# Optimization experiments

Hardware: AMD Instinct MI355X
Metric: run time of the kernel (lower is better)

The kernel has to match this reference:

```python
import jax, jax.numpy as jnp
import numpy as np

B, S, E = 4, 2048, 1024

def setup_inputs() -> dict:
    key = jax.random.key(0)
    ks = jax.random.split(key, 6)
    values = jax.random.normal(ks[0], (B, S, E), dtype=jnp.float32)
    keys_t = jax.random.normal(ks[1], (B, S, E), dtype=jnp.float32)
    query = jax.random.normal(ks[2], (B, S, E), dtype=jnp.float32)
    mask = jax.random.randint(ks[3], (B, 1, S), 0, 2, dtype=jnp.int32)
    W_out = jax.random.normal(ks[4], (E, E), dtype=jnp.float32) * (1.0 / np.sqrt(E))
    b_out = jax.random.normal(ks[5], (E,), dtype=jnp.float32) * 0.01
    return {"values": values, "keys": keys_t, "query": query, "mask": mask,
            "W_out": W_out, "b_out": b_out}

def reference(values, keys, query, mask, W_out, b_out):
    # scores: [B, S, S] = Q K^T / sqrt(embed_size)  (NOTE: module scales by
    # sqrt(embed_size), not sqrt(head_dim), and never applies q/k/v Linears)
    scale = 1.0 / jnp.sqrt(jnp.asarray(E, dtype=query.dtype))
    scores = jnp.einsum('bqe,bke->bqk', query, keys) * scale
    scores = jnp.where(mask == 0, -jnp.inf, scores)  # masked_fill(mask==0, -inf)
    attn = jax.nn.softmax(scores, axis=-1)
    out = jnp.einsum('bqk,bke->bqe', attn, values)
    # fc_out: torch Linear -> x @ W^T + b
    return out @ W_out.T + b_out
```

## Files before the change

kernel.cpp:

```cpp
#include <hip/hip_runtime.h>

#define BB 4
#define SS 2048
#define EE 1024

typedef _Float16 f16;
typedef _Float16 f16x4 __attribute__((ext_vector_type(4)));
typedef _Float16 f16x8 __attribute__((ext_vector_type(8)));
typedef float f32x4 __attribute__((ext_vector_type(4)));

typedef const __attribute__((address_space(1))) void* gas_ptr;
typedef __attribute__((address_space(3))) void* las_ptr;

__device__ __forceinline__ void gl_lds16(const void* g, void* l) {
  __builtin_amdgcn_global_load_lds((gas_ptr)g, (las_ptr)l, 16, 0, 0);
}

#define BAR() __builtin_amdgcn_s_barrier()
#define PRIO1() __builtin_amdgcn_s_setprio(1)
#define PRIO0() __builtin_amdgcn_s_setprio(0)
#define WAITV8() asm volatile("s_waitcnt vmcnt(8)" ::: "memory")
#define WAITV6() asm volatile("s_waitcnt vmcnt(6)" ::: "memory")
#define WAITV4() asm volatile("s_waitcnt vmcnt(4)" ::: "memory")
#define WAITV0() asm volatile("s_waitcnt vmcnt(0)" ::: "memory")

__global__ __launch_bounds__(256) void prep(const int* __restrict__ mask,
                                            int* __restrict__ pos,
                                            int2* __restrict__ cnt,
                                            f16* __restrict__ Kc,
                                            f16* __restrict__ Vc) {
  const int b = blockIdx.x, t = threadIdx.x;
  const int* mb = mask + b * SS;
  int4 a0 = ((const int4*)mb)[t * 2];
  int4 a1 = ((const int4*)mb)[t * 2 + 1];
  int m[8] = {a0.x, a0.y, a0.z, a0.w, a1.x, a1.y, a1.z, a1.w};
  int tot = 0;
#pragma unroll
  for (int j = 0; j < 8; ++j) tot += m[j];
  __shared__ int sc[256];
  sc[t] = tot;
  __syncthreads();
  for (int off = 1; off < 256; off <<= 1) {
    int v = (t >= off) ? sc[t - off] : 0;
    __syncthreads();
    sc[t] += v;
    __syncthreads();
  }
  const int count = sc[255];
  const int padded = (count + 127) & ~127;
  int run = sc[t] - tot;
#pragma unroll
  for (int j = 0; j < 8; ++j) {
    pos[b * SS + t * 8 + j] = run;
    run += m[j];
  }
  if (t == 0) cnt[b] = make_int2(count, padded);
  const int nz = (padded - count) * 128;
  f16x8 z = {};
  for (int i = t; i < nz; i += 256) {
    int r = count + (i >> 7), cc = i & 127;
    ((f16x8*)(Kc + ((long)b * SS + r) * EE))[cc] = z;
    ((f16x8*)(Vc + ((long)b * SS + r) * EE))[cc] = z;
  }
}

__global__ __launch_bounds__(256) void prep2(const float* __restrict__ Q,
                                             const float* __restrict__ W,
                                             const float* __restrict__ K,
                                             const float* __restrict__ V,
                                             const int* __restrict__ mask,
                                             const int* __restrict__ pos,
                                             const int2* __restrict__ cnt,
                                             f16* __restrict__ Qh,
                                             f16* __restrict__ Wh,
                                             f16* __restrict__ Kc,
                                             f16* __restrict__ Vc,
                                             float* __restrict__ rowsum,
                                             int* __restrict__ items,
                                             int* __restrict__ nit) {
  const int x = blockIdx.x, t = threadIdx.x;
  if (x < 4096) {
    const int e = x & 7, k = x >> 3;
    const int bz = e >> 1, half = e & 1, q = k >> 7, off = k & 127;
    const long logical = (long)((bz * 8 + half * 4 + q) << 7) + off;
    long i = logical * 256 + t;
    float4 v0 = ((const float4*)Q)[i * 2];
    float4 v1 = ((const float4*)Q)[i * 2 + 1];
    f16x8 o;
    o[0] = (f16)v0.x; o[1] = (f16)v0.y; o[2] = (f16)v0.z; o[3] = (f16)v0.w;
    o[4] = (f16)v1.x; o[5] = (f16)v1.y; o[6] = (f16)v1.z; o[7] = (f16)v1.w;
    ((f16x8*)Qh)[i] = o;
    return;
  }
  if (x < 4608) {
    long i = (long)(x - 4096) * 256 + t;
    float4 v0 = ((const float4*)W)[i * 2];
    float4 v1 = ((const float4*)W)[i * 2 + 1];
    f16x8 o;
    o[0] = (f16)v0.x; o[1] = (f16)v0.y; o[2] = (f16)v0.z; o[3] = (f16)v0.w;
    o[4] = (f16)v1.x; o[5] = (f16)v1.y; o[6] = (f16)v1.z; o[7] = (f16)v1.w;
    ((f16x8*)Wh)[i] = o;
    return;
  }
  if (x == 4608) {
    float4 z = {0.f, 0.f, 0.f, 0.f};
#pragma unroll
    for (int r = 0; r < 8; ++r) ((float4*)rowsum)[t + r * 256] = z;
    return;
  }
  if (x == 4609) {
    if (t < 8) {
      int nbx[4];
#pragma unroll
      for (int zz = 0; zz < 4; ++zz) nbx[zz] = (cnt[zz].y + 255) >> 8;
      int mxn = nbx[0];
#pragma unroll
      for (int zz = 1; zz < 4; ++zz) mxn = nbx[zz] > mxn ? nbx[zz] : mxn;
      const int mx = 6 * mxn;
      const int bz = t >> 1, half = t & 1;
      int g = 0;
      for (int q = 0; q < 4; ++q)
        for (int bx = 0; bx < nbx[bz]; ++bx)
          items[(g++ << 3) | t] = bx | ((half * 4 + q) << 8) | (bz << 16);
      for (int q = 0; q < 2; ++q)
        for (int bx = 0; bx < nbx[bz]; ++bx)
          items[(g++ << 3) | t] = bx | ((half * 2 + q) << 8) | (bz << 16) | (1 << 24);
      for (; g < mx; ++g) items[(g << 3) | t] = (3 << 24);
      if (t == 0) nit[0] = mx << 3;
    }
    return;
  }
  const int g = x - 4610;
  const int e = (g + 2) & 7;
  const int b = e >> 1;
  const int s = ((g >> 3) << 1) | (e & 1);
  if (!mask[b * SS + s]) return;
  const int p = pos[b * SS + s];
  float4 kv = ((const float4*)(K + ((long)b * SS + s) * EE))[t];
  float4 vv = ((const float4*)(V + ((long)b * SS + s) * EE))[t];
  f16x4 ko, vo;
  ko[0] = (f16)kv.x; ko[1] = (f16)kv.y; ko[2] = (f16)kv.z; ko[3] = (f16)kv.w;
  vo[0] = (f16)vv.x; vo[1] = (f16)vv.y; vo[2] = (f16)vv.z; vo[3] = (f16)vv.w;
  ((f16x4*)(Kc + ((long)b * SS + p) * EE))[t] = ko;
  ((f16x4*)(Vc + ((long)b * SS + p) * EE))[t] = vo;
}

__device__ __forceinline__ void stage64(const f16* g, long K, f16* l, int h, int t) {
  int rr = t >> 3, sp = t & 7;
  int row = h * 64 + rr;
  int sl = sp ^ (rr & 7);
  gl_lds16(g + (long)row * K + (sl << 3), (char*)l + ((row << 6) + (sp << 3)) * 2);
}

__device__ __forceinline__ void read_a(f16x8 (&d)[4][2], const f16* base, int q,
                                       int wm, int l15, int l4) {
#pragma unroll
  for (int mf = 0; mf < 4; ++mf)
#pragma unroll
    for (int kk = 0; kk < 2; ++kk) {
      int row = wm * 128 + (q * 4 + mf) * 16 + l15;
      int sl = kk * 4 + l4;
      d[mf][kk] = *(const f16x8*)(base + row * 64 + ((sl ^ (row & 7)) << 3));
    }
}

__device__ __forceinline__ void read_b2(f16x8 (&d)[2][2], const f16* base, int nh,
                                        int wn, int l15, int l4) {
#pragma unroll
  for (int nf = 0; nf < 2; ++nf)
#pragma unroll
    for (int kk = 0; kk < 2; ++kk) {
      int row = wn * 64 + (nh * 2 + nf) * 16 + l15;
      int sl = kk * 4 + l4;
      d[nf][kk] = *(const f16x8*)(base + row * 64 + ((sl ^ (row & 7)) << 3));
    }
}

__device__ __forceinline__ void read_b1(f16x8 (&d)[2], const f16* base, int f,
                                        int wn, int l15, int l4) {
#pragma unroll
  for (int kk = 0; kk < 2; ++kk) {
    int row = wn * 32 + f * 16 + l15;
    int sl = kk * 4 + l4;
    d[kk] = *(const f16x8*)(base + row * 64 + ((sl ^ (row & 7)) << 3));
  }
}

__device__ __forceinline__ void mfma_q(f32x4 (&acc)[8][4], const f16x8 (&Af)[4][2],
                                       const f16x8 (&Bf)[2][2], int q, int nh) {
#pragma unroll
  for (int mf = 0; mf < 4; ++mf)
#pragma unroll
    for (int nf = 0; nf < 2; ++nf)
#pragma unroll
      for (int kk = 0; kk < 2; ++kk)
        acc[q * 4 + mf][nh * 2 + nf] = __builtin_amdgcn_mfma_f32_16x16x32_f16(
            Af[mf][kk], Bf[nf][kk], acc[q * 4 + mf][nh * 2 + nf], 0, 0, 0);
}

__device__ __forceinline__ void mfma_n(f32x4 (&acc)[8][2], const f16x8 (&Af)[4][2],
                                       const f16x8 (&Bf)[2], int q, int f) {
#pragma unroll
  for (int mf = 0; mf < 4; ++mf)
#pragma unroll
    for (int kk = 0; kk < 2; ++kk)
      acc[q * 4 + mf][f] = __builtin_amdgcn_mfma_f32_16x16x32_f16(
          Af[mf][kk], Bf[kk], acc[q * 4 + mf][f], 0, 0, 0);
}

__device__ __forceinline__ void g256_core(f32x4 (&acc)[8][4], const f16* Ag,
                                          const f16* Bg, long L, int NT,
                                          f16* lds, int tid, int wm, int wn,
                                          int l15, int l4) {
  f16* As0 = lds;
  f16* As1 = lds + 16384;
  f16* Bs0 = lds + 32768;
  f16* Bs1 = lds + 49152;
  f16x8 a[4][2], b[2][2], b2[2][2];
  const int NIT = NT >> 1;

#pragma unroll
  for (int h = 0; h < 4; ++h) stage64(Bg, L, Bs0, h, tid);
#pragma unroll
  for (int h = 0; h < 4; ++h) stage64(Ag, L, As0, h, tid);
#pragma unroll
  for (int h = 0; h < 4; ++h) stage64(Bg + 64, L, Bs1, h, tid);
#pragma unroll
  for (int h = 0; h < 4; ++h) stage64(Ag + 64, L, As1, h, tid);
  WAITV8();
  BAR();

  for (int i = 0; i < NIT; ++i) {
    int t2 = 2 * i + 2, t3 = 2 * i + 3;
    long k2 = (long)((t2 < NT) ? t2 : NT - 1) << 6;
    long k3 = (long)((t3 < NT) ? t3 : NT - 1) << 6;
    read_a(a, As0, 0, wm, l15, l4);
    read_b2(b, Bs0, 0, wn, l15, l4);
    BAR(); PRIO1(); mfma_q(acc, a, b, 0, 0); PRIO0(); BAR();
    read_b2(b2, Bs0, 1, wn, l15, l4);
    BAR(); PRIO1(); mfma_q(acc, a, b2, 0, 1); PRIO0(); BAR();
    read_a(a, As0, 1, wm, l15, l4);
    stage64(Bg + k2, L, Bs0, 0, tid); stage64(Bg + k2, L, Bs0, 1, tid);
    BAR(); PRIO1(); mfma_q(acc, a, b2, 1, 1); PRIO0(); BAR();
    stage64(Bg + k2, L, Bs0, 2, tid); stage64(Bg + k2, L, Bs0, 3, tid);
    BAR(); PRIO1(); mfma_q(acc, a, b, 1, 0); PRIO0();
    WAITV4();
    BAR();
    read_a(a, As1, 0, wm, l15, l4);
    read_b2(b, Bs1, 0, wn, l15, l4);
    stage64(Ag + k2, L, As0, 0, tid); stage64(Ag + k2, L, As0, 1, tid);
    BAR(); PRIO1(); mfma_q(acc, a, b, 0, 0); PRIO0(); BAR();
    read_b2(b2, Bs1, 1, wn, l15, l4);
    stage64(Ag + k2, L, As0, 2, tid); stage64(Ag + k2, L, As0, 3, tid);
    BAR(); PRIO1(); mfma_q(acc, a, b2, 0, 1); PRIO0(); BAR();
    read_a(a, As1, 1, wm, l15, l4);
    stage64(Bg + k3, L, Bs1, 0, tid); stage64(Bg + k3, L, Bs1, 1, tid);
    BAR(); PRIO1(); mfma_q(acc, a, b2, 1, 1); PRIO0(); BAR();
    stage64(Bg + k3, L, Bs1, 2, tid); stage64(Bg + k3, L, Bs1, 3, tid);
    stage64(Ag + k3, L, As1, 0, tid); stage64(Ag + k3, L, As1, 1, tid);
    stage64(Ag + k3, L, As1, 2, tid); stage64(Ag + k3, L, As1, 3, tid);
    BAR(); PRIO1(); mfma_q(acc, a, b, 1, 0); PRIO0();
    WAITV8();
    BAR();
  }
  WAITV0();
}

__device__ __forceinline__ void n128_core(f32x4 (&acc)[8][2], const f16* Ag,
                                          const f16* Bg, long L, int NT,
                                          f16* lds, int tid, int wm, int wn,
                                          int l15, int l4) {
  f16* As0 = lds;
  f16* As1 = lds + 16384;
  f16* Bs0 = lds + 32768;
  f16* Bs1 = lds + 40960;
  f16x8 a[4][2], b[2], b2[2];
  const int NIT = NT >> 1;

  stage64(Bg, L, Bs0, 0, tid); stage64(Bg, L, Bs0, 1, tid);
#pragma unroll
  for (int h = 0; h < 4; ++h) stage64(Ag, L, As0, h, tid);
  stage64(Bg + 64, L, Bs1, 0, tid); stage64(Bg + 64, L, Bs1, 1, tid);
#pragma unroll
  for (int h = 0; h < 4; ++h) stage64(Ag + 64, L, As1, h, tid);
  WAITV6();
  BAR();

  for (int i = 0; i < NIT; ++i) {
    int t2 = 2 * i + 2, t3 = 2 * i + 3;
    long k2 = (long)((t2 < NT) ? t2 : NT - 1) << 6;
    long k3 = (long)((t3 < NT) ? t3 : NT - 1) << 6;
    read_a(a, As0, 0, wm, l15, l4);
    read_b1(b, Bs0, 0, wn, l15, l4);
    BAR(); PRIO1(); mfma_n(acc, a, b, 0, 0); PRIO0(); BAR();
    read_b1(b2, Bs0, 1, wn, l15, l4);
    BAR(); PRIO1(); mfma_n(acc, a, b2, 0, 1); PRIO0(); BAR();
    read_a(a, As0, 1, wm, l15, l4);
    stage64(Bg + k2, L, Bs0, 0, tid); stage64(Bg + k2, L, Bs0, 1, tid);
    BAR(); PRIO1(); mfma_n(acc, a, b2, 1, 1); PRIO0(); BAR();
#pragma unroll
    for (int h = 0; h < 4; ++h) stage64(Ag + k2, L, As0, h, tid);
    BAR(); PRIO1(); mfma_n(acc, a, b, 1, 0); PRIO0();
    WAITV6();
    BAR();
    read_a(a, As1, 0, wm, l15, l4);
    read_b1(b, Bs1, 0, wn, l15, l4);
    BAR(); PRIO1(); mfma_n(acc, a, b, 0, 0); PRIO0(); BAR();
    read_b1(b2, Bs1, 1, wn, l15, l4);
    BAR(); PRIO1(); mfma_n(acc, a, b2, 0, 1); PRIO0(); BAR();
    read_a(a, As1, 1, wm, l15, l4);
    stage64(Bg + k3, L, Bs1, 0, tid); stage64(Bg + k3, L, Bs1, 1, tid);
    BAR(); PRIO1(); mfma_n(acc, a, b2, 1, 1); PRIO0(); BAR();
#pragma unroll
    for (int h = 0; h < 4; ++h) stage64(Ag + k3, L, As1, h, tid);
    BAR(); PRIO1(); mfma_n(acc, a, b, 1, 0); PRIO0();
    WAITV6();
    BAR();
  }
  WAITV0();
}

__global__ __launch_bounds__(512, 1) void uber(const f16* __restrict__ Qh,
                                               const f16* __restrict__ Kc,
                                               const f16* __restrict__ Vc,
                                               const f16* __restrict__ Wh,
                                               f16* __restrict__ P,
                                               f16* __restrict__ VWt,
                                               float* __restrict__ rowsum,
                                               const int2* __restrict__ cnt,
                                               const int* __restrict__ items,
                                               const int* __restrict__ nit) {
  extern __shared__ f16 lds[];
  const int tid = threadIdx.x;
  const int lane = tid & 63, wv = tid >> 6;
  const int wm = wv >> 2, wn = wv & 3;
  const int l15 = lane & 15, l4 = lane >> 4;
  const int n = nit[0];

  for (int idx = blockIdx.x; idx < n; idx += 256) {
    const int it = items[idx];
    const int kind = (it >> 24) & 3;
    if (kind == 3) continue;
    const int bx = it & 255, by = (it >> 8) & 255, bz = (it >> 16) & 255;
    const long m0 = (long)by * 256;
    const long n0 = (long)bx * 256;
    const f16* Ag = kind ? (Wh + m0 * EE) : (Qh + (long)bz * SS * EE + m0 * EE);
    const f16* Bg = (kind ? Vc : Kc) + (long)bz * SS * EE + n0 * EE;

    f32x4 acc[8][4] = {};
    g256_core(acc, Ag, Bg, EE, EE >> 6, lds, tid, wm, wn, l15, l4);

    const long crow = m0 + wm * 128 + l4 * 4;
    const long ccol = n0 + wn * 64 + l15;
    if (kind == 0) {
      const int count = cnt[bz].x;
      f16* Co = P + (long)bz * SS * SS;
      float* rs = rowsum + (bz << 11);
      const float scale = 1.0f / 32.0f;
      int mv[4];
#pragma unroll
      for (int nf = 0; nf < 4; ++nf) mv[nf] = (ccol + nf * 16) < count;
#pragma unroll
      for (int mf = 0; mf < 8; ++mf)
#pragma unroll
        for (int jj = 0; jj < 4; ++jj) {
          float rp = 0.f;
#pragma unroll
          for (int nf = 0; nf < 4; ++nf) {
            float p = mv[nf] ? __expf(acc[mf][nf][jj] * scale) : 0.f;
            Co[(crow + mf * 16 + jj) * SS + ccol + nf * 16] = (f16)p;
            rp += p;
          }
          rp += __shfl_xor(rp, 1); rp += __shfl_xor(rp, 2);
          rp += __shfl_xor(rp, 4); rp += __shfl_xor(rp, 8);
          if (l15 == 0) atomicAdd(&rs[crow + mf * 16 + jj], rp);
        }
    } else {
      f16* Co = VWt + (long)bz * EE * SS;
#pragma unroll
      for (int mf = 0; mf < 8; ++mf)
#pragma unroll
        for (int nf = 0; nf < 4; ++nf)
#pragma unroll
          for (int jj = 0; jj < 4; ++jj)
            Co[(crow + mf * 16 + jj) * SS + ccol + nf * 16] = (f16)acc[mf][nf][jj];
    }
  }
}

__global__ __launch_bounds__(512, 1) void pv128(const f16* __restrict__ P,
                                                const f16* __restrict__ VWt,
                                                float* __restrict__ out,
                                                const float* __restrict__ bias,
                                                const float* __restrict__ rowsum,
                                                const int2* __restrict__ cnt) {
  extern __shared__ f16 lds[];
  const int d = blockIdx.x;
  const int x = d & 7, r = d >> 3;
  const int bz = x >> 1;
  const int by = (x & 1) * 4 + (r & 3);
  const int bx = r >> 2;
  int2 cc = cnt[bz];
  const int padded = cc.y;
  if (padded <= 0) return;
  const long m0 = (long)by * 256;
  const long n0 = (long)bx * 128;
  const int tid = threadIdx.x;
  const int lane = tid & 63, wv = tid >> 6;
  const int wm = wv >> 2, wn = wv & 3;
  const int l15 = lane & 15, l4 = lane >> 4;
  const f16* Ag = P + (long)bz * SS * SS + m0 * SS;
  const f16* Bg = VWt + (long)bz * EE * SS + n0 * SS;

  f32x4 acc[8][2] = {};
  n128_core(acc, Ag, Bg, SS, padded >> 6, lds, tid, wm, wn, l15, l4);

  const long crow = m0 + wm * 128 + l4 * 4;
  const long ccol = n0 + wn * 32 + l15;
  float* Co = out + (long)bz * SS * EE;
  const float* rs = rowsum + (bz << 11);
  float bv[2];
#pragma unroll
  for (int nf = 0; nf < 2; ++nf) bv[nf] = bias[ccol + nf * 16];
#pragma unroll
  for (int mf = 0; mf < 8; ++mf)
#pragma unroll
    for (int jj = 0; jj < 4; ++jj) {
      float inv = 1.f / rs[crow + mf * 16 + jj];
#pragma unroll
      for (int nf = 0; nf < 2; ++nf)
        Co[(crow + mf * 16 + jj) * EE + ccol + nf * 16] =
            acc[mf][nf][jj] * inv + bv[nf];
    }
}

extern "C" void kernel_launch(void* const* d_in, const int* in_sizes, int n_in,
                              void* d_out, int out_size, void* d_ws, size_t ws_size,
                              hipStream_t stream) {
  const float* V = (const float*)d_in[0];
  const float* Kin = (const float*)d_in[1];
  const float* Q = (const float*)d_in[2];
  const int* mask = (const int*)d_in[3];
  const float* W = (const float*)d_in[4];
  const float* bias = (const float*)d_in[5];
  float* out = (float*)d_out;

  const long NE = (long)BB * SS * EE;
  f16* Qh = (f16*)d_ws;
  f16* Kc = Qh + NE;
  f16* Vc = Kc + NE;
  f16* Wh = Vc + NE;
  f16* VWt = Wh + (long)EE * EE;
  f16* P = VWt + NE;
  float* rowsum = (float*)(P + (long)BB * SS * SS);
  int* pos = (int*)(rowsum + (long)BB * SS);
  int2* cnt = (int2*)(pos + (long)BB * SS);
  int* items = (int*)(cnt + BB);
  int* nit = items + 1024;

  const size_t LDS_Q = 131072, LDS_N = 98304;
  hipFuncSetAttribute((const void*)uber, hipFuncAttributeMaxDynamicSharedMemorySize, LDS_Q);
  hipFuncSetAttribute((const void*)pv128, hipFuncAttributeMaxDynamicSharedMemorySize, LDS_N);

  prep<<<BB, 256, 0, stream>>>(mask, pos, cnt, Kc, Vc);
  prep2<<<4610 + BB * SS, 256, 0, stream>>>(Q, W, Kin, V, mask, pos, cnt,
                                            Qh, Wh, Kc, Vc, rowsum, items, nit);
  uber<<<256, 512, LDS_Q, stream>>>(Qh, Kc, Vc, Wh, P, VWt, rowsum, cnt, items, nit);
  pv128<<<256, 512, LDS_N, stream>>>(P, VWt, out, bias, rowsum, cnt);
}
```

Measured before the change: 91.70 us.

## Fuse PV GEMM into persistent uber kernel with per-tile completion counters

Merges the separate PV kernel into the persistent uber kernel as a third round of work items, gated by atomic per-row-block counters that QK and WV tiles increment after storing. This removes the launch gap and tail between the two GEMM phases so PV tiles can start as soon as their inputs are ready. It also simplifies the prep index orderings and fixes the item count at 512 slots. The spin-wait on counters risks deadlock if producer blocks are not resident, and padding items no longer depend on the max count.

```diff
diff --git a/kernel.cpp b/kernel.cpp
--- a/kernel.cpp
+++ b/kernel.cpp
@@ -77,13 +77,10 @@
                                              f16* __restrict__ Vc,
                                              float* __restrict__ rowsum,
                                              int* __restrict__ items,
-                                             int* __restrict__ nit) {
+                                             int* __restrict__ done) {
   const int x = blockIdx.x, t = threadIdx.x;
   if (x < 4096) {
-    const int e = x & 7, k = x >> 3;
-    const int bz = e >> 1, half = e & 1, q = k >> 7, off = k & 127;
-    const long logical = (long)((bz * 8 + half * 4 + q) << 7) + off;
-    long i = logical * 256 + t;
+    long i = (long)x * 256 + t;
     float4 v0 = ((const float4*)Q)[i * 2];
     float4 v1 = ((const float4*)Q)[i * 2 + 1];
     f16x8 o;
@@ -106,6 +103,7 @@
     float4 z = {0.f, 0.f, 0.f, 0.f};
 #pragma unroll
     for (int r = 0; r < 8; ++r) ((float4*)rowsum)[t + r * 256] = z;
+    if (t < 48) done[t] = 0;
     return;
   }
   if (x == 4609) {
@@ -113,10 +111,6 @@
       int nbx[4];
 #pragma unroll
       for (int zz = 0; zz < 4; ++zz) nbx[zz] = (cnt[zz].y + 255) >> 8;
-      int mxn = nbx[0];
-#pragma unroll
-      for (int zz = 1; zz < 4; ++zz) mxn = nbx[zz] > mxn ? nbx[zz] : mxn;
-      const int mx = 6 * mxn;
       const int bz = t >> 1, half = t & 1;
       int g = 0;
       for (int q = 0; q < 4; ++q)
@@ -125,15 +119,11 @@
       for (int q = 0; q < 2; ++q)
         for (int bx = 0; bx < nbx[bz]; ++bx)
           items[(g++ << 3) | t] = bx | ((half * 2 + q) << 8) | (bz << 16) | (1 << 24);
-      for (; g < mx; ++g) items[(g << 3) | t] = (3 << 24);
-      if (t == 0) nit[0] = mx << 3;
+      for (; g < 64; ++g) items[(g << 3) | t] = (3 << 24);
     }
     return;
   }
-  const int g = x - 4610;
-  const int e = (g + 2) & 7;
-  const int b = e >> 1;
-  const int s = ((g >> 3) << 1) | (e & 1);
+  const int g = x - 4610, b = g >> 11, s = g & (SS - 1);
   if (!mask[b * SS + s]) return;
   const int p = pos[b * SS + s];
   float4 kv = ((const float4*)(K + ((long)b * SS + s) * EE))[t];
@@ -326,112 +316,121 @@
                                                const f16* __restrict__ Wh,
                                                f16* __restrict__ P,
                                                f16* __restrict__ VWt,
+                                               float* __restrict__ out,
+                                               const float* __restrict__ bias,
                                                float* __restrict__ rowsum,
                                                const int2* __restrict__ cnt,
                                                const int* __restrict__ items,
-                                               const int* __restrict__ nit) {
+                                               int* __restrict__ done) {
   extern __shared__ f16 lds[];
   const int tid = threadIdx.x;
   const int lane = tid & 63, wv = tid >> 6;
   const int wm = wv >> 2, wn = wv & 3;
   const int l15 = lane & 15, l4 = lane >> 4;
-  const int n = nit[0];
-
-  for (int idx = blockIdx.x; idx < n; idx += 256) {
-    const int it = items[idx];
-    const int kind = (it >> 24) & 3;
-    if (kind == 3) continue;
-    const int bx = it & 255, by = (it >> 8) & 255, bz = (it >> 16) & 255;
-    const long m0 = (long)by * 256;
-    const long n0 = (long)bx * 256;
-    const f16* Ag = kind ? (Wh + m0 * EE) : (Qh + (long)bz * SS * EE + m0 * EE);
-    const f16* Bg = (kind ? Vc : Kc) + (long)bz * SS * EE + n0 * EE;
-
-    f32x4 acc[8][4] = {};
-    g256_core(acc, Ag, Bg, EE, EE >> 6, lds, tid, wm, wn, l15, l4);
-
-    const long crow = m0 + wm * 128 + l4 * 4;
-    const long ccol = n0 + wn * 64 + l15;
-    if (kind == 0) {
-      const int count = cnt[bz].x;
-      f16* Co = P + (long)bz * SS * SS;
-      float* rs = rowsum + (bz << 11);
-      const float scale = 1.0f / 32.0f;
-      int mv[4];
-#pragma unroll
-      for (int nf = 0; nf < 4; ++nf) mv[nf] = (ccol + nf * 16) < count;
+  int* doneQK = done;
+  int* doneWV = done + 32;
+
+  for (int idx = blockIdx.x; idx < 768; idx += 256) {
+    if (idx < 512) {
+      const int it = items[idx];
+      const int kind = (it >> 24) & 3;
+      if (kind == 3) continue;
+      const int bx = it & 255, by = (it >> 8) & 255, bz = (it >> 16) & 255;
+      const long m0 = (long)by * 256;
+      const long n0 = (long)bx * 256;
+      const f16* Ag = kind ? (Wh + m0 * EE) : (Qh + (long)bz * SS * EE + m0 * EE);
+      const f16* Bg = (kind ? Vc : Kc) + (long)bz * SS * EE + n0 * EE;
+
+      f32x4 acc[8][4] = {};
+      g256_core(acc, Ag, Bg, EE, EE >> 6, lds, tid, wm, wn, l15, l4);
+
+      const long crow = m0 + wm * 128 + l4 * 4;
+      const long ccol = n0 + wn * 64 + l15;
+      if (kind == 0) {
+        const int count = cnt[bz].x;
+        f16* Co = P + (long)bz * SS * SS;
+        float* rs = rowsum + (bz << 11);
+        const float scale = 1.0f / 32.0f;
+        int mv[4];
+#pragma unroll
+        for (int nf = 0; nf < 4; ++nf) mv[nf] = (ccol + nf * 16) < count;
+#pragma unroll
+        for (int mf = 0; mf < 8; ++mf)
+#pragma unroll
+          for (int jj = 0; jj < 4; ++jj) {
+            float rp = 0.f;
+#pragma unroll
+            for (int nf = 0; nf < 4; ++nf) {
+              float p = mv[nf] ? __expf(acc[mf][nf][jj] * scale) : 0.f;
+              Co[(crow + mf * 16 + jj) * SS + ccol + nf * 16] = (f16)p;
+              rp += p;
+            }
+            rp += __shfl_xor(rp, 1); rp += __shfl_xor(rp, 2);
+            rp += __shfl_xor(rp, 4); rp += __shfl_xor(rp, 8);
+            if (l15 == 0) atomicAdd(&rs[crow + mf * 16 + jj], rp);
+          }
+        __threadfence();
+        BAR();
+        if (tid == 0) atomicAdd(&doneQK[bz * 8 + by], 1);
+      } else {
+        f16* Co = VWt + (long)bz * EE * SS;
+#pragma unroll
+        for (int mf = 0; mf < 8; ++mf)
+#pragma unroll
+          for (int nf = 0; nf < 4; ++nf)
+#pragma unroll
+            for (int jj = 0; jj < 4; ++jj)
+              Co[(crow + mf * 16 + jj) * SS + ccol + nf * 16] = (f16)acc[mf][nf][jj];
+        __threadfence();
+        BAR();
+        if (tid == 0) atomicAdd(&doneWV[bz * 4 + by], 1);
+      }
+    } else {
+      const int d = idx - 512;
+      const int x = d & 7, r = d >> 3;
+      const int bz = x >> 1;
+      const int by = (x & 1) * 4 + (r & 3);
+      const int bx = r >> 2;
+      const int2 cc = cnt[bz];
+      const int need = (cc.y + 255) >> 8;
+      if (tid == 0) {
+        while (__hip_atomic_load(&doneQK[bz * 8 + by], __ATOMIC_RELAXED,
+                                 __HIP_MEMORY_SCOPE_AGENT) < need)
+          __builtin_amdgcn_s_sleep(8);
+        while (__hip_atomic_load(&doneWV[bz * 4 + (bx >> 1)], __ATOMIC_RELAXED,
+                                 __HIP_MEMORY_SCOPE_AGENT) < need)
+          __builtin_amdgcn_s_sleep(8);
+      }
+      BAR();
+      __threadfence();
+
+      const long m0 = (long)by * 256;
+      const long n0 = (long)bx * 128;
+      const f16* Ag = P + (long)bz * SS * SS + m0 * SS;
+      const f16* Bg = VWt + (long)bz * EE * SS + n0 * SS;
+
+      f32x4 acc[8][2] = {};
+      n128_core(acc, Ag, Bg, SS, cc.y >> 6, lds, tid, wm, wn, l15, l4);
+
+      const long crow = m0 + wm * 128 + l4 * 4;
+      const long ccol = n0 + wn * 32 + l15;
+      float* Co = out + (long)bz * SS * EE;
+      const float* rs = rowsum + (bz << 11);
+      float bv[2];
+#pragma unroll
+      for (int nf = 0; nf < 2; ++nf) bv[nf] = bias[ccol + nf * 16];
 #pragma unroll
       for (int mf = 0; mf < 8; ++mf)
 #pragma unroll
         for (int jj = 0; jj < 4; ++jj) {
-          float rp = 0.f;
-#pragma unroll
-          for (int nf = 0; nf < 4; ++nf) {
-            float p = mv[nf] ? __expf(acc[mf][nf][jj] * scale) : 0.f;
-            Co[(crow + mf * 16 + jj) * SS + ccol + nf * 16] = (f16)p;
-            rp += p;
-          }
-          rp += __shfl_xor(rp, 1); rp += __shfl_xor(rp, 2);
-          rp += __shfl_xor(rp, 4); rp += __shfl_xor(rp, 8);
-          if (l15 == 0) atomicAdd(&rs[crow + mf * 16 + jj], rp);
+          float inv = 1.f / rs[crow + mf * 16 + jj];
+#pragma unroll
+          for (int nf = 0; nf < 2; ++nf)
+            Co[(crow + mf * 16 + jj) * EE + ccol + nf * 16] =
+                acc[mf][nf][jj] * inv + bv[nf];
         }
-    } else {
-      f16* Co = VWt + (long)bz * EE * SS;
-#pragma unroll
-      for (int mf = 0; mf < 8; ++mf)
-#pragma unroll
-        for (int nf = 0; nf < 4; ++nf)
-#pragma unroll
-          for (int jj = 0; jj < 4; ++jj)
-            Co[(crow + mf * 16 + jj) * SS + ccol + nf * 16] = (f16)acc[mf][nf][jj];
     }
   }
-}
-
-__global__ __launch_bounds__(512, 1) void pv128(const f16* __restrict__ P,
-                                                const f16* __restrict__ VWt,
-                                                float* __restrict__ out,
-                                                const float* __restrict__ bias,
-                                                const float* __restrict__ rowsum,
-                                                const int2* __restrict__ cnt) {
-  extern __shared__ f16 lds[];
-  const int d = blockIdx.x;
-  const int x = d & 7, r = d >> 3;
-  const int bz = x >> 1;
-  const int by = (x & 1) * 4 + (r & 3);
-  const int bx = r >> 2;
-  int2 cc = cnt[bz];
-  const int padded = cc.y;
-  if (padded <= 0) return;
-  const long m0 = (long)by * 256;
-  const long n0 = (long)bx * 128;
-  const int tid = threadIdx.x;
-  const int lane = tid & 63, wv = tid >> 6;
-  const int wm = wv >> 2, wn = wv & 3;
-  const int l15 = lane & 15, l4 = lane >> 4;
-  const f16* Ag = P + (long)bz * SS * SS + m0 * SS;
-  const f16* Bg = VWt + (long)bz * EE * SS + n0 * SS;
-
-  f32x4 acc[8][2] = {};
-  n128_core(acc, Ag, Bg, SS, padded >> 6, lds, tid, wm, wn, l15, l4);
-
-  const long crow = m0 + wm * 128 + l4 * 4;
-  const long ccol = n0 + wn * 32 + l15;
-  float* Co = out + (long)bz * SS * EE;
-  const float* rs = rowsum + (bz << 11);
-  float bv[2];
-#pragma unroll
-  for (int nf = 0; nf < 2; ++nf) bv[nf] = bias[ccol + nf * 16];
-#pragma unroll
-  for (int mf = 0; mf < 8; ++mf)
-#pragma unroll
-    for (int jj = 0; jj < 4; ++jj) {
-      float inv = 1.f / rs[crow + mf * 16 + jj];
-#pragma unroll
-      for (int nf = 0; nf < 2; ++nf)
-        Co[(crow + mf * 16 + jj) * EE + ccol + nf * 16] =
-            acc[mf][nf][jj] * inv + bv[nf];
-    }
 }
 
 extern "C" void kernel_launch(void* const* d_in, const int* in_sizes, int n_in,
@@ -456,15 +455,14 @@
   int* pos = (int*)(rowsum + (long)BB * SS);
   int2* cnt = (int2*)(pos + (long)BB * SS);
   int* items = (int*)(cnt + BB);
-  int* nit = items + 1024;
-
-  const size_t LDS_Q = 131072, LDS_N = 98304;
+  int* done = items + 1024;
+
+  const size_t LDS_Q = 131072;
   hipFuncSetAttribute((const void*)uber, hipFuncAttributeMaxDynamicSharedMemorySize, LDS_Q);
-  hipFuncSetAttribute((const void*)pv128, hipFuncAttributeMaxDynamicSharedMemorySize, LDS_N);
 
   prep<<<BB, 256, 0, stream>>>(mask, pos, cnt, Kc, Vc);
   prep2<<<4610 + BB * SS, 256, 0, stream>>>(Q, W, Kin, V, mask, pos, cnt,
-                                            Qh, Wh, Kc, Vc, rowsum, items, nit);
-  uber<<<256, 512, LDS_Q, stream>>>(Qh, Kc, Vc, Wh, P, VWt, rowsum, cnt, items, nit);
-  pv128<<<256, 512, LDS_N, stream>>>(P, VWt, out, bias, rowsum, cnt);
-}
+                                            Qh, Wh, Kc, Vc, rowsum, items, done);
+  uber<<<256, 512, LDS_Q, stream>>>(Qh, Kc, Vc, Wh, P, VWt, out, bias, rowsum,
+                                    cnt, items, done);
+}
```

Result: slower. 192.7 us (+110.2%).
